# Performance work log

Measured on AMD Instinct MI355X. Metric: run time of the kernel, lower is better.

Reference implementation:

```python
import jax, jax.numpy as jnp
import numpy as np
from jax import lax

DIM = 96
B, H, W = 4, 256, 256


def setup_inputs() -> dict:
    key = jax.random.key(0)
    ks = jax.random.split(key, 20)
    f = lambda k, s, scale=0.05: (jax.random.normal(k, s, dtype=jnp.float32) * scale)
    d = DIM
    return {
        "x": jax.random.normal(ks[0], (B, d, H, W), dtype=jnp.float32),
        "prompt": jax.random.normal(ks[1], (B, d), dtype=jnp.float32),
        "scale_weights": jax.random.uniform(ks[2], (B, 3), dtype=jnp.float32),
        "ln_w": jnp.ones((d,), jnp.float32),
        "ln_b": jnp.zeros((d,), jnp.float32),
        "e0_pw_w": f(ks[3], (d, d)),       # expert0 pointwise 1x1: [out, in]
        "e0_pw_b": f(ks[4], (d,)),
        "e0_dw_w": f(ks[5], (d, 1, 3, 3)),  # depthwise 3x3
        "e0_dw_b": f(ks[6], (d,)),
        "e1_dw_w": f(ks[7], (d, 1, 3, 3)),  # depthwise 3x3, dilation 2
        "e1_dw_b": f(ks[8], (d,)),
        "e2_dw_w": f(ks[9], (d, 1, 5, 5)),  # depthwise 5x5, dilation 3
        "e2_dw_b": f(ks[10], (d,)),
        "proj_w": f(ks[11], (d, d)),
        "proj_b": f(ks[12], (d,)),
        "ffn1_w": f(ks[13], (2 * d, d)),
        "ffn1_b": f(ks[14], (2 * d,)),
        "ffn2_w": f(ks[15], (d, 2 * d)),
        "ffn2_b": f(ks[16], (d,)),
    }


def _conv1x1(x, w, b):
    # x: [B,C,H,W], w: [O,C]
    return jnp.einsum('bchw,oc->bohw', x, w) + b[None, :, None, None]


def _dwconv(x, w, b, dilation, pad):
    # depthwise conv, w: [C,1,k,k]
    c = x.shape[1]
    y = lax.conv_general_dilated(
        x, w, window_strides=(1, 1),
        padding=[(pad, pad), (pad, pad)],
        rhs_dilation=(dilation, dilation),
        feature_group_count=c,
        dimension_numbers=('NCHW', 'OIHW', 'NCHW'))
    return y + b[None, :, None, None]


def _layernorm_c(x, w, b, eps=1e-6):
    # LayerNorm over channel dim of NCHW (torch permutes to NHWC, norms last dim)
    mu = jnp.mean(x, axis=1, keepdims=True)
    var = jnp.mean((x - mu) ** 2, axis=1, keepdims=True)
    xn = (x - mu) * lax.rsqrt(var + eps)
    return xn * w[None, :, None, None] + b[None, :, None, None]


def reference(x, prompt, scale_weights, ln_w, ln_b,
              e0_pw_w, e0_pw_b, e0_dw_w, e0_dw_b,
              e1_dw_w, e1_dw_b, e2_dw_w, e2_dw_b,
              proj_w, proj_b, ffn1_w, ffn1_b, ffn2_w, ffn2_b):
    shortcut = x
    xn = _layernorm_c(x, ln_w, ln_b)

    # Three receptive-field experts (all run densely, soft-weighted)
    e0 = _dwconv(_conv1x1(xn, e0_pw_w, e0_pw_b), e0_dw_w, e0_dw_b, dilation=1, pad=1)
    e1 = _dwconv(xn, e1_dw_w, e1_dw_b, dilation=2, pad=2)
    e2 = _dwconv(xn, e2_dw_w, e2_dw_b, dilation=3, pad=6)

    w = scale_weights  # [B,3]
    x_adaptive = (w[:, 0, None, None, None] * e0
                  + w[:, 1, None, None, None] * e1
                  + w[:, 2, None, None, None] * e2)
    x_adaptive = x_adaptive * (1.0 + prompt[:, :, None, None])

    x1 = shortcut + _conv1x1(x_adaptive, proj_w, proj_b)
    h = jax.nn.gelu(_conv1x1(x1, ffn1_w, ffn1_b), approximate=False)
    out = x1 + _conv1x1(h, ffn2_w, ffn2_b)
    return out
```

## Files before the change

### kernel.cpp

```cpp
#include <hip/hip_runtime.h>
#include <hip/hip_bf16.h>

typedef __hip_bfloat16 bf16;
typedef __attribute__((ext_vector_type(8))) __bf16 bf16x8;
typedef __attribute__((ext_vector_type(4))) float  f32x4;

#define HW   65536
#define WID  256
#define CC   96
#define NB   4
static const size_t S_ELEMS = (size_t)NB * CC * HW;

__device__ __forceinline__ float lo2f(unsigned u) { unsigned x = u << 16;        return __builtin_bit_cast(float, x); }
__device__ __forceinline__ float hi2f(unsigned u) { unsigned x = u & 0xffff0000u; return __builtin_bit_cast(float, x); }
__device__ __forceinline__ unsigned short f2bu(float f) {
    return __builtin_bit_cast(unsigned short, __float2bfloat16(f));
}

__device__ __forceinline__ float gelu_erf(float v) {
    float z  = fabsf(v) * 0.70710678118654752f;
    float t  = __builtin_amdgcn_rcpf(1.f + 0.3275911f * z);
    float poly = t * (0.254829592f + t * (-0.284496736f + t * (1.421413741f
               + t * (-1.453152027f + t * 1.061405429f))));
    float erfz = 1.f - poly * __expf(-z * z);
    float erfv = copysignf(erfz, v);
    return 0.5f * v * (1.f + erfv);
}

__global__ __launch_bounds__(256) void ln_kernel(
    const float* __restrict__ x, const float* __restrict__ lw,
    const float* __restrict__ lb, bf16* __restrict__ y)
{
    int t  = blockIdx.x * 256 + threadIdx.x;
    int b  = t >> 15;
    int hw = (t & 32767) * 2;
    size_t base = (size_t)b * CC * HW + hw;

    float s0 = 0.f, s1 = 0.f, q0 = 0.f, q1 = 0.f;
    for (int c = 0; c < CC; ++c) {
        float2 v = *reinterpret_cast<const float2*>(&x[base + (size_t)c * HW]);
        s0 += v.x; s1 += v.y; q0 += v.x * v.x; q1 += v.y * v.y;
    }
    float mu0 = s0 * (1.f / 96.f), mu1 = s1 * (1.f / 96.f);
    float rs0 = rsqrtf(q0 * (1.f / 96.f) - mu0 * mu0 + 1e-6f);
    float rs1 = rsqrtf(q1 * (1.f / 96.f) - mu1 * mu1 + 1e-6f);

    for (int c = 0; c < CC; ++c) {
        float2 v = *reinterpret_cast<const float2*>(&x[base + (size_t)c * HW]);
        float g = lw[c], be = lb[c];
        bf16 o[2];
        o[0] = __float2bfloat16((v.x - mu0) * rs0 * g + be);
        o[1] = __float2bfloat16((v.y - mu1) * rs1 * g + be);
        *reinterpret_cast<uint*>(&y[base + (size_t)c * HW]) = *reinterpret_cast<uint*>(o);
    }
}

__device__ __forceinline__ int swzo(int row, int col, int width) {
    return (row * width + col) ^ ((((row & 7) ^ ((row >> 3) & 7)) << 3));
}

template <typename TI, typename TOT, int CIN, int COUT, bool GELU, bool HASRES>
__global__ __launch_bounds__(256) void conv1x1_mfma(
    const TI* __restrict__ in, const float* __restrict__ wgt,
    const float* __restrict__ bias, const float* __restrict__ resid,
    TOT* __restrict__ out)
{
    constexpr int KSPLIT = CIN / 96;
    constexpr int OSPLIT = COUT / 96;
    constexpr int MT     = 6;
    static_assert(CIN == KSPLIT * 96 && COUT == OSPLIT * 96, "96-multiples only");

    __shared__ unsigned short s_w[96 * 96];
    __shared__ unsigned short s_x[128 * 96];
    __shared__ float          s_b[COUT];

    const int tid  = threadIdx.x;
    const int lane = tid & 63;
    const int wave = tid >> 6;
    const int q    = lane >> 4;
    const int n    = lane & 15;

    const int pos0 = blockIdx.x * 128;
    const int b    = pos0 >> 16;
    const int hw0  = pos0 & 65535;

    for (int k = tid; k < COUT; k += 256) s_b[k] = bias[k];

    const TI* inb = in + (size_t)b * CIN * HW;
    const int pl0 = wave * 32 + n;
    const int pl1 = pl0 + 16;

#pragma unroll
    for (int os = 0; os < OSPLIT; ++os) {
        f32x4 acc[MT][2];
#pragma unroll
        for (int mt = 0; mt < MT; ++mt) {
            acc[mt][0] = {0.f, 0.f, 0.f, 0.f};
            acc[mt][1] = {0.f, 0.f, 0.f, 0.f};
        }

#pragma unroll
        for (int ks = 0; ks < KSPLIT; ++ks) {
            for (int k = tid; k < 96 * 24; k += 256) {
                int o = k / 24, c4 = (k - o * 24) * 4;
                float4 w4 = *reinterpret_cast<const float4*>(
                    &wgt[(size_t)(os * 96 + o) * CIN + ks * 96 + c4]);
                ushort4 pk = make_ushort4(f2bu(w4.x), f2bu(w4.y), f2bu(w4.z), f2bu(w4.w));
                *reinterpret_cast<ushort4*>(&s_w[swzo(o, c4, 96)]) = pk;
            }
            if (KSPLIT > 1 || os == 0) {
                for (int idx = tid; idx < 48 * 16; idx += 256) {
                    const int cp = idx >> 4;
                    const int pb = idx & 15;
                    const TI* gp = inb + (size_t)(ks * 96 + 2 * cp) * HW + hw0 + pb * 8;
                    unsigned short ua[8], ub[8];
                    if constexpr (__is_same(TI, float)) {
                        float4 a0 = *reinterpret_cast<const float4*>(gp);
                        float4 a1 = *reinterpret_cast<const float4*>(gp + 4);
                        float4 b0 = *reinterpret_cast<const float4*>(gp + HW);
                        float4 b1 = *reinterpret_cast<const float4*>(gp + HW + 4);
                        ua[0]=f2bu(a0.x); ua[1]=f2bu(a0.y); ua[2]=f2bu(a0.z); ua[3]=f2bu(a0.w);
                        ua[4]=f2bu(a1.x); ua[5]=f2bu(a1.y); ua[6]=f2bu(a1.z); ua[7]=f2bu(a1.w);
                        ub[0]=f2bu(b0.x); ub[1]=f2bu(b0.y); ub[2]=f2bu(b0.z); ub[3]=f2bu(b0.w);
                        ub[4]=f2bu(b1.x); ub[5]=f2bu(b1.y); ub[6]=f2bu(b1.z); ub[7]=f2bu(b1.w);
                    } else {
                        *reinterpret_cast<uint4*>(ua) = *reinterpret_cast<const uint4*>(gp);
                        *reinterpret_cast<uint4*>(ub) = *reinterpret_cast<const uint4*>(gp + HW);
                    }
#pragma unroll
                    for (int i = 0; i < 8; ++i) {
                        uint d = (uint)ua[i] | ((uint)ub[i] << 16);
                        *reinterpret_cast<uint*>(&s_x[swzo(pb * 8 + i, 2 * cp, 96)]) = d;
                    }
                }
            }
            __syncthreads();

#pragma unroll
            for (int kt = 0; kt < 3; ++kt) {
                const int col = kt * 32 + q * 8;
                union { unsigned short u[8]; bf16x8 v; } bf0, bf1;
                *reinterpret_cast<uint4*>(bf0.u) =
                    *reinterpret_cast<const uint4*>(&s_x[swzo(pl0, col, 96)]);
                *reinterpret_cast<uint4*>(bf1.u) =
                    *reinterpret_cast<const uint4*>(&s_x[swzo(pl1, col, 96)]);
#pragma unroll
                for (int mt = 0; mt < MT; ++mt) {
                    union { unsigned short u[8]; bf16x8 v; } fa;
                    *reinterpret_cast<uint4*>(fa.u) =
                        *reinterpret_cast<const uint4*>(&s_w[swzo(mt * 16 + n, col, 96)]);
                    acc[mt][0] = __builtin_amdgcn_mfma_f32_16x16x32_bf16(fa.v, bf0.v, acc[mt][0], 0, 0, 0);
                    acc[mt][1] = __builtin_amdgcn_mfma_f32_16x16x32_bf16(fa.v, bf1.v, acc[mt][1], 0, 0, 0);
                }
            }
            if (os + 1 < OSPLIT || ks + 1 < KSPLIT)
                __syncthreads();
        }

        const int p0 = hw0 + pl0;
        const int p1 = hw0 + pl1;
        const size_t obase = (size_t)b * COUT * HW;
#pragma unroll
        for (int mt = 0; mt < MT; ++mt) {
#pragma unroll
            for (int nt = 0; nt < 2; ++nt) {
                const int p = (nt == 0) ? p0 : p1;
#pragma unroll
                for (int r = 0; r < 4; ++r) {
                    const int o = os * 96 + mt * 16 + q * 4 + r;
                    float v = acc[mt][nt][r] + s_b[o];
                    if constexpr (GELU) v = gelu_erf(v);
                    const size_t idx = obase + (size_t)o * HW + p;
                    if constexpr (HASRES) v += resid[idx];
                    if constexpr (__is_same(TOT, float)) out[idx] = v;
                    else                                 out[idx] = __float2bfloat16(v);
                }
            }
        }
    }
}

__global__ __launch_bounds__(512, 2) void ffn_fused(
    const bf16* __restrict__ xa, const float* __restrict__ x,
    const float* __restrict__ pw, const float* __restrict__ pb,
    const float* __restrict__ w1, const float* __restrict__ b1,
    const float* __restrict__ w2, const float* __restrict__ b2,
    float* __restrict__ out)
{
    __shared__ unsigned short s_w[96 * 96];
    __shared__ unsigned short s_x1[128 * 96];
    __shared__ unsigned short s_hx[128 * 96];
    __shared__ float          s_bias[384];

    const int tid  = threadIdx.x;
    const int lane = tid & 63;
    const int w8   = tid >> 6;
    const int q    = lane >> 4;
    const int n    = lane & 15;

    const int pos0 = blockIdx.x * 128;
    const int b    = pos0 >> 16;
    const int hw0  = pos0 & 65535;
    const int pl   = w8 * 16 + n;
    const int p    = hw0 + pl;

    ushort4 wrp[5];
    auto WLOAD = [&](const float* W, int row0, int col0, int rs) {
        float4 t[5];
#pragma unroll
        for (int i = 0; i < 5; ++i) {
            const int idx = tid + i * 512;
            if (i < 4 || tid < 256) {
                const int o = idx / 24, c4 = (idx - o * 24) * 4;
                t[i] = *reinterpret_cast<const float4*>(
                    &W[(size_t)(row0 + o) * rs + col0 + c4]);
            }
        }
#pragma unroll
        for (int i = 0; i < 5; ++i)
            if (i < 4 || tid < 256)
                wrp[i] = make_ushort4(f2bu(t[i].x), f2bu(t[i].y),
                                      f2bu(t[i].z), f2bu(t[i].w));
    };
    auto WWRITE = [&]() {
#pragma unroll
        for (int i = 0; i < 5; ++i) {
            const int idx = tid + i * 512;
            if (i < 4 || tid < 256) {
                const int o = idx / 24, c4 = (idx - o * 24) * 4;
                *reinterpret_cast<ushort4*>(&s_w[swzo(o, c4, 96)]) = wrp[i];
            }
        }
    };
    auto GEMM = [&](const unsigned short* B, f32x4 (&acc)[6]) {
#pragma unroll
        for (int kt = 0; kt < 3; ++kt) {
            const int col = kt * 32 + q * 8;
            union { unsigned short u[8]; bf16x8 v; } bf;
            *reinterpret_cast<uint4*>(bf.u) =
                *reinterpret_cast<const uint4*>(&B[swzo(pl, col, 96)]);
#pragma unroll
            for (int mt = 0; mt < 6; ++mt) {
                union { unsigned short u[8]; bf16x8 v; } fa;
                *reinterpret_cast<uint4*>(fa.u) =
                    *reinterpret_cast<const uint4*>(&s_w[swzo(mt * 16 + n, col, 96)]);
                acc[mt] = __builtin_amdgcn_mfma_f32_16x16x32_bf16(fa.v, bf.v, acc[mt], 0, 0, 0);
            }
        }
    };
    auto ST4 = [&](unsigned short* dst, int col4, float v0, float v1, float v2, float v3) {
        union { unsigned short u[4]; uint2 d; } t;
        t.u[0] = f2bu(v0); t.u[1] = f2bu(v1); t.u[2] = f2bu(v2); t.u[3] = f2bu(v3);
        *reinterpret_cast<uint2*>(&dst[swzo(pl, col4, 96)]) = t.d;
    };

    {
        const bf16* inb = xa + (size_t)b * 96 * HW;
        for (int idx = tid; idx < 48 * 16; idx += 512) {
            const int cp = idx >> 4, pbk = idx & 15;
            const bf16* gp = inb + (size_t)(2 * cp) * HW + hw0 + pbk * 8;
            unsigned short ua[8], ub[8];
            *reinterpret_cast<uint4*>(ua) = *reinterpret_cast<const uint4*>(gp);
            *reinterpret_cast<uint4*>(ub) = *reinterpret_cast<const uint4*>(gp + HW);
#pragma unroll
            for (int i = 0; i < 8; ++i) {
                uint d = (uint)ua[i] | ((uint)ub[i] << 16);
                *reinterpret_cast<uint*>(&s_hx[swzo(pbk * 8 + i, 2 * cp, 96)]) = d;
            }
        }
        for (int k = tid; k < 96 * 24; k += 512) {
            const int o = k / 24, c4 = (k - o * 24) * 4;
            float4 w4 = *reinterpret_cast<const float4*>(&pw[(size_t)o * 96 + c4]);
            ushort4 pk = make_ushort4(f2bu(w4.x), f2bu(w4.y), f2bu(w4.z), f2bu(w4.w));
            *reinterpret_cast<ushort4*>(&s_w[swzo(o, c4, 96)]) = pk;
        }
        if (tid < 96)  s_bias[tid]       = pb[tid];
        if (tid < 192) s_bias[96 + tid]  = b1[tid];
        if (tid < 96)  s_bias[288 + tid] = b2[tid];
    }
    __syncthreads();

    WLOAD(w1, 0, 0, 96);
    float xr[6][4];
    {
        const size_t xbase = (size_t)b * 96 * HW;
#pragma unroll
        for (int mt = 0; mt < 6; ++mt)
#pragma unroll
            for (int r = 0; r < 4; ++r)
                xr[mt][r] = x[xbase + (size_t)(mt * 16 + q * 4 + r) * HW + p];
    }
    float x1f[6][4];
    {
        f32x4 accp[6];
#pragma unroll
        for (int mt = 0; mt < 6; ++mt) accp[mt] = {0.f, 0.f, 0.f, 0.f};
        GEMM(s_hx, accp);
#pragma unroll
        for (int mt = 0; mt < 6; ++mt) {
#pragma unroll
            for (int r = 0; r < 4; ++r)
                x1f[mt][r] = accp[mt][r] + s_bias[mt * 16 + q * 4 + r] + xr[mt][r];
            ST4(s_x1, mt * 16 + q * 4, x1f[mt][0], x1f[mt][1], x1f[mt][2], x1f[mt][3]);
        }
    }
    __syncthreads();

    WWRITE();
    __syncthreads();

    WLOAD(w2, 0, 0, 192);
    {
        f32x4 a1[6];
#pragma unroll
        for (int mt = 0; mt < 6; ++mt) a1[mt] = {0.f, 0.f, 0.f, 0.f};
        GEMM(s_x1, a1);
#pragma unroll
        for (int mt = 0; mt < 6; ++mt) {
            float v0 = gelu_erf(a1[mt][0] + s_bias[96 + mt * 16 + q * 4 + 0]);
            float v1 = gelu_erf(a1[mt][1] + s_bias[96 + mt * 16 + q * 4 + 1]);
            float v2 = gelu_erf(a1[mt][2] + s_bias[96 + mt * 16 + q * 4 + 2]);
            float v3 = gelu_erf(a1[mt][3] + s_bias[96 + mt * 16 + q * 4 + 3]);
            ST4(s_hx, mt * 16 + q * 4, v0, v1, v2, v3);
        }
    }
    __syncthreads();

    WWRITE();
    __syncthreads();

    f32x4 acc2[6];
#pragma unroll
    for (int mt = 0; mt < 6; ++mt) acc2[mt] = {0.f, 0.f, 0.f, 0.f};
    WLOAD(w1, 96, 0, 96);
    GEMM(s_hx, acc2);
    __syncthreads();

    WWRITE();
    __syncthreads();

    WLOAD(w2, 0, 96, 192);
    {
        f32x4 a1[6];
#pragma unroll
        for (int mt = 0; mt < 6; ++mt) a1[mt] = {0.f, 0.f, 0.f, 0.f};
        GEMM(s_x1, a1);
#pragma unroll
        for (int mt = 0; mt < 6; ++mt) {
            float v0 = gelu_erf(a1[mt][0] + s_bias[192 + mt * 16 + q * 4 + 0]);
            float v1 = gelu_erf(a1[mt][1] + s_bias[192 + mt * 16 + q * 4 + 1]);
            float v2 = gelu_erf(a1[mt][2] + s_bias[192 + mt * 16 + q * 4 + 2]);
            float v3 = gelu_erf(a1[mt][3] + s_bias[192 + mt * 16 + q * 4 + 3]);
            ST4(s_hx, mt * 16 + q * 4, v0, v1, v2, v3);
        }
    }
    __syncthreads();

    WWRITE();
    __syncthreads();

    GEMM(s_hx, acc2);
    {
        const size_t obase = (size_t)b * 96 * HW;
#pragma unroll
        for (int mt = 0; mt < 6; ++mt)
#pragma unroll
            for (int r = 0; r < 4; ++r) {
                const int o = mt * 16 + q * 4 + r;
                out[obase + (size_t)o * HW + p] = x1f[mt][r] + acc2[mt][r] + s_bias[288 + o];
            }
    }
}

#define XR     20
#define XPITCH 22
#define TPITCH 10
#define XCOLS  268
#define TCOLS  258

__global__ __launch_bounds__(256) void experts_kernel(
    const bf16* __restrict__ xn, const bf16* __restrict__ t0,
    const float* __restrict__ w0, const float* __restrict__ b0,
    const float* __restrict__ w1, const float* __restrict__ b1,
    const float* __restrict__ w2, const float* __restrict__ b2,
    const float* __restrict__ sw, const float* __restrict__ prompt,
    bf16* __restrict__ xa)
{
    __shared__ alignas(16) unsigned short sxT[XCOLS * XPITCH];
    __shared__ alignas(16) unsigned short stT[TCOLS * TPITCH];

    const int tid  = threadIdx.x;
    const int lane = tid & 63;
    const int wave = tid >> 6;
    const int bid = blockIdx.x;
    const int h0  = (bid & 31) * 8;
    const int bc  = bid >> 5;
    const int b   = bc / 96;
    const int c   = bc - b * 96;
    const size_t pbase = (size_t)bc * HW;

    const bf16* xp = xn + pbase;
    const bf16* tp = t0 + pbase;
    uint* sx32 = reinterpret_cast<uint*>(sxT);
    uint* st32 = reinterpret_cast<uint*>(stT);

    if (tid < 132) {
        int cc = tid / 11, d = tid - cc * 11;
        int col = (cc < 6) ? cc : 256 + cc;
        sx32[col * 11 + d] = 0u;
    } else if (tid < 142) {
        int i = tid - 132;
        int col = (i < 5) ? 0 : 257;
        int d   = (i < 5) ? i : i - 5;
        st32[col * 5 + d] = 0u;
    }

    {
        const int rp = (lane >> 2) & 7;
        const int ch = 8 * wave + (lane & 3) + ((lane >> 5) << 2);
        const int gh0 = h0 - 6 + 2 * rp, gh1 = gh0 + 1;
        union { uint4 q; unsigned short u[8]; } a, bb;
        a.q  = ((unsigned)gh0 < 256u) ? *reinterpret_cast<const uint4*>(xp + gh0 * WID + ch * 8)
                                      : make_uint4(0u, 0u, 0u, 0u);
        bb.q = ((unsigned)gh1 < 256u) ? *reinterpret_cast<const uint4*>(xp + gh1 * WID + ch * 8)
                                      : make_uint4(0u, 0u, 0u, 0u);
        const int base = 11 * (6 + 8 * ch) + rp;
#pragma unroll
        for (int j = 0; j < 8; ++j)
            sx32[base + 11 * j] = (uint)a.u[j] | ((uint)bb.u[j] << 16);
    }
    if (wave == 2) {
        const int rp = 8 + ((lane >> 2) & 1);
        const int ch = (lane & 3) + (((lane >> 3) & 7) << 2);
        const int gh0 = h0 - 6 + 2 * rp, gh1 = gh0 + 1;
        union { uint4 q; unsigned short u[8]; } a, bb;
        a.q  = ((unsigned)gh0 < 256u) ? *reinterpret_cast<const uint4*>(xp + gh0 * WID + ch * 8)
                                      : make_uint4(0u, 0u, 0u, 0u);
        bb.q = ((unsigned)gh1 < 256u) ? *reinterpret_cast<const uint4*>(xp + gh1 * WID + ch * 8)
                                      : make_uint4(0u, 0u, 0u, 0u);
        const int base = 11 * (6 + 8 * ch) + rp;
#pragma unroll
        for (int j = 0; j < 8; ++j)
            sx32[base + 11 * j] = (uint)a.u[j] | ((uint)bb.u[j] << 16);
    }
    if (wave < 2) {
        const int rp = (lane >> 3) & 3;
        const int ch = 16 * wave + (lane & 7) + ((lane >> 5) << 3);
        const int gh0 = h0 - 1 + 2 * rp, gh1 = gh0 + 1;
        union { uint4 q; unsigned short u[8]; } a, bb;
        a.q  = ((unsigned)gh0 < 256u) ? *reinterpret_cast<const uint4*>(tp + gh0 * WID + ch * 8)
                                      : make_uint4(0u, 0u, 0u, 0u);
        bb.q = ((unsigned)gh1 < 256u) ? *reinterpret_cast<const uint4*>(tp + gh1 * WID + ch * 8)
                                      : make_uint4(0u, 0u, 0u, 0u);
        const int base = 5 * (1 + 8 * ch) + rp;
#pragma unroll
        for (int j = 0; j < 8; ++j)
            st32[base + 5 * j] = (uint)a.u[j] | ((uint)bb.u[j] << 16);
    }
    if (wave == 3 && lane < 32) {
        const int rp = 4;
        const int ch = lane;
        const int gh0 = h0 - 1 + 2 * rp, gh1 = gh0 + 1;
        union { uint4 q; unsigned short u[8]; } a, bb;
        a.q  = ((unsigned)gh0 < 256u) ? *reinterpret_cast<const uint4*>(tp + gh0 * WID + ch * 8)
                                      : make_uint4(0u, 0u, 0u, 0u);
        bb.q = ((unsigned)gh1 < 256u) ? *reinterpret_cast<const uint4*>(tp + gh1 * WID + ch * 8)
                                      : make_uint4(0u, 0u, 0u, 0u);
        const int base = 5 * (1 + 8 * ch) + rp;
#pragma unroll
        for (int j = 0; j < 8; ++j)
            st32[base + 5 * j] = (uint)a.u[j] | ((uint)bb.u[j] << 16);
    }

    float wk0[9], wk1[9], wk2[25];
#pragma unroll
    for (int i = 0; i < 9; ++i)  wk0[i] = w0[c * 9 + i];
#pragma unroll
    for (int i = 0; i < 9; ++i)  wk1[i] = w1[c * 9 + i];
#pragma unroll
    for (int i = 0; i < 25; ++i) wk2[i] = w2[c * 25 + i];
    const float bb0 = b0[c], bb1 = b1[c], bb2 = b2[c];
    const float s0 = sw[b * 3 + 0], s1 = sw[b * 3 + 1], s2 = sw[b * 3 + 2];
    const float pr = 1.f + prompt[b * 96 + c];

    __syncthreads();

    const int w = tid;
    float acc0[8], acc1[8], acc2[8];
#pragma unroll
    for (int r = 0; r < 8; ++r) { acc0[r] = bb0; acc1[r] = bb1; acc2[r] = bb2; }

    const unsigned short* bx = &sxT[w * XPITCH];
    const unsigned short* bt = &stT[w * TPITCH];

#pragma unroll
    for (int kw = 0; kw < 5; ++kw) {
        float cv[20];
#pragma unroll
        for (int j = 0; j < 10; ++j) {
            unsigned u = *reinterpret_cast<const unsigned*>(&bx[kw * 3 * XPITCH + 2 * j]);
            cv[2 * j]     = lo2f(u);
            cv[2 * j + 1] = hi2f(u);
        }
#pragma unroll
        for (int kh = 0; kh < 5; ++kh) {
            const float wv = wk2[kh * 5 + kw];
#pragma unroll
            for (int r = 0; r < 8; ++r) acc2[r] += wv * cv[r + 3 * kh];
        }
        if (kw == 2) {
#pragma unroll
            for (int kh = 0; kh < 3; ++kh) {
                const float wv = wk1[kh * 3 + 1];
#pragma unroll
                for (int r = 0; r < 8; ++r) acc1[r] += wv * cv[r + 2 * kh + 4];
            }
        }
    }
#pragma unroll
    for (int kwh = 0; kwh < 2; ++kwh) {
        const int kw = kwh * 2;
        float cv[12];
#pragma unroll
        for (int j = 0; j < 6; ++j) {
            unsigned u = *reinterpret_cast<const unsigned*>(&bx[(4 + 2 * kw) * XPITCH + 4 + 2 * j]);
            cv[2 * j]     = lo2f(u);
            cv[2 * j + 1] = hi2f(u);
        }
#pragma unroll
        for (int kh = 0; kh < 3; ++kh) {
            const float wv = wk1[kh * 3 + kw];
#pragma unroll
            for (int r = 0; r < 8; ++r) acc1[r] += wv * cv[r + 2 * kh];
        }
    }
#pragma unroll
    for (int kw = 0; kw < 3; ++kw) {
        float cv[10];
#pragma unroll
        for (int j = 0; j < 5; ++j) {
            unsigned u = *reinterpret_cast<const unsigned*>(&bt[kw * TPITCH + 2 * j]);
            cv[2 * j]     = lo2f(u);
            cv[2 * j + 1] = hi2f(u);
        }
#pragma unroll
        for (int kh = 0; kh < 3; ++kh) {
            const float wv = wk0[kh * 3 + kw];
#pragma unroll
            for (int r = 0; r < 8; ++r) acc0[r] += wv * cv[r + kh];
        }
    }

    bf16* op = xa + pbase + (size_t)h0 * WID + w;
#pragma unroll
    for (int r = 0; r < 8; ++r) {
        float v = (s0 * acc0[r] + s1 * acc1[r] + s2 * acc2[r]) * pr;
        op[r * WID] = __float2bfloat16(v);
    }
}

extern "C" void kernel_launch(void* const* d_in, const int* in_sizes, int n_in,
                              void* d_out, int out_size, void* d_ws, size_t ws_size,
                              hipStream_t stream)
{
    const float* x       = (const float*)d_in[0];
    const float* prompt  = (const float*)d_in[1];
    const float* sw      = (const float*)d_in[2];
    const float* ln_w    = (const float*)d_in[3];
    const float* ln_b    = (const float*)d_in[4];
    const float* e0_pw_w = (const float*)d_in[5];
    const float* e0_pw_b = (const float*)d_in[6];
    const float* e0_dw_w = (const float*)d_in[7];
    const float* e0_dw_b = (const float*)d_in[8];
    const float* e1_dw_w = (const float*)d_in[9];
    const float* e1_dw_b = (const float*)d_in[10];
    const float* e2_dw_w = (const float*)d_in[11];
    const float* e2_dw_b = (const float*)d_in[12];
    const float* proj_w  = (const float*)d_in[13];
    const float* proj_b  = (const float*)d_in[14];
    const float* ffn1_w  = (const float*)d_in[15];
    const float* ffn1_b  = (const float*)d_in[16];
    const float* ffn2_w  = (const float*)d_in[17];
    const float* ffn2_b  = (const float*)d_in[18];

    float* out = (float*)d_out;
    bf16*  ws  = (bf16*)d_ws;
    bf16*  A   = ws;
    bf16*  Bt  = ws + S_ELEMS;
    bf16*  Cx  = ws + 2 * S_ELEMS;

    ln_kernel<<<512, 256, 0, stream>>>(x, ln_w, ln_b, A);
    conv1x1_mfma<bf16, bf16, 96, 96, false, false>
        <<<2048, 256, 0, stream>>>(A, e0_pw_w, e0_pw_b, nullptr, Bt);
    experts_kernel<<<12288, 256, 0, stream>>>(A, Bt, e0_dw_w, e0_dw_b, e1_dw_w, e1_dw_b,
                                              e2_dw_w, e2_dw_b, sw, prompt, Cx);
    ffn_fused<<<2048, 512, 0, stream>>>(Cx, x, proj_w, proj_b,
                                        ffn1_w, ffn1_b, ffn2_w, ffn2_b, out);
}
```

Baseline: 425.5 us.

## Rework layernorm thread mapping and specialize expert pointwise conv with staged stores

The layernorm kernel now gives each pixel to two threads that each hold 48 channels in registers. Their statistics are combined with a lane shuffle, so x is read only once instead of twice, and the grid has more blocks. The generic templated 1x1 conv is replaced by a specialized 96->96 kernel with 64-pixel tiles and an occupancy hint. Its bf16 results are staged through shared memory so global stores are 16-byte vectors instead of scalar 2-byte writes. The costs are higher register pressure from the 48-value array and more LDS passes and barriers.

```diff
diff --git a/kernel.cpp b/kernel.cpp
--- a/kernel.cpp
+++ b/kernel.cpp
@@ -31,27 +31,36 @@
     const float* __restrict__ x, const float* __restrict__ lw,
     const float* __restrict__ lb, bf16* __restrict__ y)
 {
-    int t  = blockIdx.x * 256 + threadIdx.x;
-    int b  = t >> 15;
-    int hw = (t & 32767) * 2;
-    size_t base = (size_t)b * CC * HW + hw;
-
-    float s0 = 0.f, s1 = 0.f, q0 = 0.f, q1 = 0.f;
-    for (int c = 0; c < CC; ++c) {
-        float2 v = *reinterpret_cast<const float2*>(&x[base + (size_t)c * HW]);
-        s0 += v.x; s1 += v.y; q0 += v.x * v.x; q1 += v.y * v.y;
-    }
-    float mu0 = s0 * (1.f / 96.f), mu1 = s1 * (1.f / 96.f);
-    float rs0 = rsqrtf(q0 * (1.f / 96.f) - mu0 * mu0 + 1e-6f);
-    float rs1 = rsqrtf(q1 * (1.f / 96.f) - mu1 * mu1 + 1e-6f);
-
-    for (int c = 0; c < CC; ++c) {
-        float2 v = *reinterpret_cast<const float2*>(&x[base + (size_t)c * HW]);
-        float g = lw[c], be = lb[c];
-        bf16 o[2];
-        o[0] = __float2bfloat16((v.x - mu0) * rs0 * g + be);
-        o[1] = __float2bfloat16((v.y - mu1) * rs1 * g + be);
-        *reinterpret_cast<uint*>(&y[base + (size_t)c * HW]) = *reinterpret_cast<uint*>(o);
+    __shared__ float s_g[96], s_be[96];
+    const int tid = threadIdx.x;
+    if (tid < 96)  s_g[tid]  = lw[tid];
+    else if (tid >= 128 && tid < 224) s_be[tid - 128] = lb[tid - 128];
+    __syncthreads();
+
+    const int t  = blockIdx.x * 256 + tid;
+    const int p  = t >> 1;
+    const int h  = t & 1;
+    const int b  = p >> 16;
+    const int hw = p & 65535;
+    const float* xp = x + (size_t)b * CC * HW + hw + (size_t)(h * 48) * HW;
+
+    float v[48];
+    float s = 0.f, q = 0.f;
+#pragma unroll
+    for (int i = 0; i < 48; ++i) {
+        v[i] = xp[(size_t)i * HW];
+        s += v[i]; q += v[i] * v[i];
+    }
+    s += __shfl_xor(s, 1);
+    q += __shfl_xor(q, 1);
+    const float mu = s * (1.f / 96.f);
+    const float rs = rsqrtf(q * (1.f / 96.f) - mu * mu + 1e-6f);
+
+    bf16* yp = y + (size_t)b * CC * HW + hw + (size_t)(h * 48) * HW;
+#pragma unroll
+    for (int i = 0; i < 48; ++i) {
+        const int c = h * 48 + i;
+        yp[(size_t)i * HW] = __float2bfloat16((v[i] - mu) * rs * s_g[c] + s_be[c]);
     }
 }
 
@@ -59,20 +68,13 @@
     return (row * width + col) ^ ((((row & 7) ^ ((row >> 3) & 7)) << 3));
 }
 
-template <typename TI, typename TOT, int CIN, int COUT, bool GELU, bool HASRES>
-__global__ __launch_bounds__(256) void conv1x1_mfma(
-    const TI* __restrict__ in, const float* __restrict__ wgt,
-    const float* __restrict__ bias, const float* __restrict__ resid,
-    TOT* __restrict__ out)
+__global__ __launch_bounds__(256, 5) void conv96_kernel(
+    const bf16* __restrict__ in, const float* __restrict__ wgt,
+    const float* __restrict__ bias, bf16* __restrict__ out)
 {
-    constexpr int KSPLIT = CIN / 96;
-    constexpr int OSPLIT = COUT / 96;
-    constexpr int MT     = 6;
-    static_assert(CIN == KSPLIT * 96 && COUT == OSPLIT * 96, "96-multiples only");
-
     __shared__ unsigned short s_w[96 * 96];
-    __shared__ unsigned short s_x[128 * 96];
-    __shared__ float          s_b[COUT];
+    __shared__ unsigned short s_x[64 * 96];
+    __shared__ float          s_b[96];
 
     const int tid  = threadIdx.x;
     const int lane = tid & 63;
@@ -80,103 +82,73 @@
     const int q    = lane >> 4;
     const int n    = lane & 15;
 
-    const int pos0 = blockIdx.x * 128;
+    const int pos0 = blockIdx.x * 64;
     const int b    = pos0 >> 16;
     const int hw0  = pos0 & 65535;
-
-    for (int k = tid; k < COUT; k += 256) s_b[k] = bias[k];
-
-    const TI* inb = in + (size_t)b * CIN * HW;
-    const int pl0 = wave * 32 + n;
-    const int pl1 = pl0 + 16;
-
-#pragma unroll
-    for (int os = 0; os < OSPLIT; ++os) {
-        f32x4 acc[MT][2];
-#pragma unroll
-        for (int mt = 0; mt < MT; ++mt) {
-            acc[mt][0] = {0.f, 0.f, 0.f, 0.f};
-            acc[mt][1] = {0.f, 0.f, 0.f, 0.f};
-        }
-
-#pragma unroll
-        for (int ks = 0; ks < KSPLIT; ++ks) {
-            for (int k = tid; k < 96 * 24; k += 256) {
-                int o = k / 24, c4 = (k - o * 24) * 4;
-                float4 w4 = *reinterpret_cast<const float4*>(
-                    &wgt[(size_t)(os * 96 + o) * CIN + ks * 96 + c4]);
-                ushort4 pk = make_ushort4(f2bu(w4.x), f2bu(w4.y), f2bu(w4.z), f2bu(w4.w));
-                *reinterpret_cast<ushort4*>(&s_w[swzo(o, c4, 96)]) = pk;
-            }
-            if (KSPLIT > 1 || os == 0) {
-                for (int idx = tid; idx < 48 * 16; idx += 256) {
-                    const int cp = idx >> 4;
-                    const int pb = idx & 15;
-                    const TI* gp = inb + (size_t)(ks * 96 + 2 * cp) * HW + hw0 + pb * 8;
-                    unsigned short ua[8], ub[8];
-                    if constexpr (__is_same(TI, float)) {
-                        float4 a0 = *reinterpret_cast<const float4*>(gp);
-                        float4 a1 = *reinterpret_cast<const float4*>(gp + 4);
-                        float4 b0 = *reinterpret_cast<const float4*>(gp + HW);
-                        float4 b1 = *reinterpret_cast<const float4*>(gp + HW + 4);
-                        ua[0]=f2bu(a0.x); ua[1]=f2bu(a0.y); ua[2]=f2bu(a0.z); ua[3]=f2bu(a0.w);
-                        ua[4]=f2bu(a1.x); ua[5]=f2bu(a1.y); ua[6]=f2bu(a1.z); ua[7]=f2bu(a1.w);
-                        ub[0]=f2bu(b0.x); ub[1]=f2bu(b0.y); ub[2]=f2bu(b0.z); ub[3]=f2bu(b0.w);
-                        ub[4]=f2bu(b1.x); ub[5]=f2bu(b1.y); ub[6]=f2bu(b1.z); ub[7]=f2bu(b1.w);
-                    } else {
-                        *reinterpret_cast<uint4*>(ua) = *reinterpret_cast<const uint4*>(gp);
-                        *reinterpret_cast<uint4*>(ub) = *reinterpret_cast<const uint4*>(gp + HW);
-                    }
-#pragma unroll
-                    for (int i = 0; i < 8; ++i) {
-                        uint d = (uint)ua[i] | ((uint)ub[i] << 16);
-                        *reinterpret_cast<uint*>(&s_x[swzo(pb * 8 + i, 2 * cp, 96)]) = d;
-                    }
-                }
-            }
-            __syncthreads();
-
-#pragma unroll
-            for (int kt = 0; kt < 3; ++kt) {
-                const int col = kt * 32 + q * 8;
-                union { unsigned short u[8]; bf16x8 v; } bf0, bf1;
-                *reinterpret_cast<uint4*>(bf0.u) =
-                    *reinterpret_cast<const uint4*>(&s_x[swzo(pl0, col, 96)]);
-                *reinterpret_cast<uint4*>(bf1.u) =
-                    *reinterpret_cast<const uint4*>(&s_x[swzo(pl1, col, 96)]);
-#pragma unroll
-                for (int mt = 0; mt < MT; ++mt) {
-                    union { unsigned short u[8]; bf16x8 v; } fa;
-                    *reinterpret_cast<uint4*>(fa.u) =
-                        *reinterpret_cast<const uint4*>(&s_w[swzo(mt * 16 + n, col, 96)]);
-                    acc[mt][0] = __builtin_amdgcn_mfma_f32_16x16x32_bf16(fa.v, bf0.v, acc[mt][0], 0, 0, 0);
-                    acc[mt][1] = __builtin_amdgcn_mfma_f32_16x16x32_bf16(fa.v, bf1.v, acc[mt][1], 0, 0, 0);
-                }
-            }
-            if (os + 1 < OSPLIT || ks + 1 < KSPLIT)
-                __syncthreads();
-        }
-
-        const int p0 = hw0 + pl0;
-        const int p1 = hw0 + pl1;
-        const size_t obase = (size_t)b * COUT * HW;
-#pragma unroll
-        for (int mt = 0; mt < MT; ++mt) {
-#pragma unroll
-            for (int nt = 0; nt < 2; ++nt) {
-                const int p = (nt == 0) ? p0 : p1;
-#pragma unroll
-                for (int r = 0; r < 4; ++r) {
-                    const int o = os * 96 + mt * 16 + q * 4 + r;
-                    float v = acc[mt][nt][r] + s_b[o];
-                    if constexpr (GELU) v = gelu_erf(v);
-                    const size_t idx = obase + (size_t)o * HW + p;
-                    if constexpr (HASRES) v += resid[idx];
-                    if constexpr (__is_same(TOT, float)) out[idx] = v;
-                    else                                 out[idx] = __float2bfloat16(v);
-                }
-            }
-        }
+    const size_t cbase = (size_t)b * CC * HW + hw0;
+
+    if (tid < 96) s_b[tid] = bias[tid];
+
+    for (int k = tid; k < 96 * 24; k += 256) {
+        const int o = k / 24, c4 = (k - o * 24) * 4;
+        float4 w4 = *reinterpret_cast<const float4*>(&wgt[o * 96 + c4]);
+        ushort4 pk = make_ushort4(f2bu(w4.x), f2bu(w4.y), f2bu(w4.z), f2bu(w4.w));
+        *reinterpret_cast<ushort4*>(&s_w[swzo(o, c4, 96)]) = pk;
+    }
+    const bf16* inb = in + cbase;
+    for (int idx = tid; idx < 384; idx += 256) {
+        const int cp  = idx >> 3;
+        const int pbk = idx & 7;
+        const bf16* gp = inb + (size_t)(2 * cp) * HW + pbk * 8;
+        union { uint4 v; unsigned short u[8]; } a, c;
+        a.v = *reinterpret_cast<const uint4*>(gp);
+        c.v = *reinterpret_cast<const uint4*>(gp + HW);
+#pragma unroll
+        for (int i = 0; i < 8; ++i)
+            *reinterpret_cast<uint*>(&s_x[swzo(pbk * 8 + i, 2 * cp, 96)]) =
+                (uint)a.u[i] | ((uint)c.u[i] << 16);
+    }
+    __syncthreads();
+
+    const int pl = wave * 16 + n;
+    f32x4 acc[6];
+#pragma unroll
+    for (int mt = 0; mt < 6; ++mt) acc[mt] = {0.f, 0.f, 0.f, 0.f};
+#pragma unroll
+    for (int kt = 0; kt < 3; ++kt) {
+        const int col = kt * 32 + q * 8;
+        union { unsigned short u[8]; bf16x8 v; } bf;
+        *reinterpret_cast<uint4*>(bf.u) =
+            *reinterpret_cast<const uint4*>(&s_x[swzo(pl, col, 96)]);
+#pragma unroll
+        for (int mt = 0; mt < 6; ++mt) {
+            union { unsigned short u[8]; bf16x8 v; } fa;
+            *reinterpret_cast<uint4*>(fa.u) =
+                *reinterpret_cast<const uint4*>(&s_w[swzo(mt * 16 + n, col, 96)]);
+            acc[mt] = __builtin_amdgcn_mfma_f32_16x16x32_bf16(fa.v, bf.v, acc[mt], 0, 0, 0);
+        }
+    }
+    __syncthreads();
+
+#pragma unroll
+    for (int mt = 0; mt < 6; ++mt) {
+        const int o0 = mt * 16 + q * 4;
+        union { unsigned short u[4]; uint2 d; } t4;
+        t4.u[0] = f2bu(acc[mt][0] + s_b[o0 + 0]);
+        t4.u[1] = f2bu(acc[mt][1] + s_b[o0 + 1]);
+        t4.u[2] = f2bu(acc[mt][2] + s_b[o0 + 2]);
+        t4.u[3] = f2bu(acc[mt][3] + s_b[o0 + 3]);
+        *reinterpret_cast<uint2*>(&s_x[swzo(pl, o0, 96)]) = t4.d;
+    }
+    __syncthreads();
+
+    for (int idx = tid; idx < 768; idx += 256) {
+        const int ch = idx >> 3, pbk = idx & 7;
+        alignas(16) unsigned short u[8];
+#pragma unroll
+        for (int i = 0; i < 8; ++i) u[i] = s_x[swzo(pbk * 8 + i, ch, 96)];
+        *reinterpret_cast<uint4*>(&out[cbase + (size_t)ch * HW + pbk * 8]) =
+            *reinterpret_cast<const uint4*>(u);
     }
 }
 
@@ -589,9 +561,8 @@
     bf16*  Bt  = ws + S_ELEMS;
     bf16*  Cx  = ws + 2 * S_ELEMS;
 
-    ln_kernel<<<512, 256, 0, stream>>>(x, ln_w, ln_b, A);
-    conv1x1_mfma<bf16, bf16, 96, 96, false, false>
-        <<<2048, 256, 0, stream>>>(A, e0_pw_w, e0_pw_b, nullptr, Bt);
+    ln_kernel<<<2048, 256, 0, stream>>>(x, ln_w, ln_b, A);
+    conv96_kernel<<<4096, 256, 0, stream>>>(A, e0_pw_w, e0_pw_b, Bt);
     experts_kernel<<<12288, 256, 0, stream>>>(A, Bt, e0_dw_w, e0_dw_b, e1_dw_w, e1_dw_b,
                                               e2_dw_w, e2_dw_b, sw, prompt, Cx);
     ffn_fused<<<2048, 512, 0, stream>>>(Cx, x, proj_w, proj_b,
```

Result: no change. 425.8 us (+0.1%).
